# Kernel optimization log

Hardware: AMD Instinct MI355X
Metric: run time of the kernel (lower is better)

Reference implementation:

```python
import jax, jax.numpy as jnp
import numpy as np

DIM = 1024
NUM_HEADS = 16
HEAD_DIM = DIM // NUM_HEADS
BATCH = 2
SEQ = 2048
ROPE_BASE = 10000.0


def _rope_cos_sin(seq_len, head_dim, dtype=jnp.float32):
    inv_freq = 1.0 / (ROPE_BASE ** (jnp.arange(0, head_dim, 2, dtype=jnp.float32) / head_dim))
    t = jnp.arange(seq_len, dtype=jnp.float32)
    freqs = jnp.outer(t, inv_freq)              # (S, D/2)
    emb = jnp.concatenate([freqs, freqs], axis=-1)  # (S, D)
    return jnp.cos(emb).astype(dtype), jnp.sin(emb).astype(dtype)


def _rotate_half(x):
    x1, x2 = jnp.split(x, 2, axis=-1)
    return jnp.concatenate([-x2, x1], axis=-1)


def _apply_rope(x, cos, sin):
    # x: (B, S, H, D); cos/sin: (S, D) -> broadcast (1, S, 1, D)
    cos = cos[None, :, None, :]
    sin = sin[None, :, None, :]
    return x * cos + _rotate_half(x) * sin


def setup_inputs() -> dict:
    key = jax.random.key(0)
    ks = jax.random.split(key, 5)
    x = jax.random.normal(ks[0], (BATCH, SEQ, DIM), dtype=jnp.float32)
    scale = DIM ** -0.5
    wq = jax.random.normal(ks[1], (DIM, DIM), dtype=jnp.float32) * scale
    wk = jax.random.normal(ks[2], (DIM, DIM), dtype=jnp.float32) * scale
    wv = jax.random.normal(ks[3], (DIM, DIM), dtype=jnp.float32) * scale
    wo = jax.random.normal(ks[4], (DIM, DIM), dtype=jnp.float32) * scale
    return {"x": x, "wq": wq, "wk": wk, "wv": wv, "wo": wo}


def reference(x, wq, wk, wv, wo):
    B, S, _ = x.shape
    scale = HEAD_DIM ** -0.5
    # nn.Linear(x) = x @ W.T; weights stored (out, in)
    q = (x @ wq.T).reshape(B, S, NUM_HEADS, HEAD_DIM)
    k = (x @ wk.T).reshape(B, S, NUM_HEADS, HEAD_DIM)
    v = (x @ wv.T).reshape(B, S, NUM_HEADS, HEAD_DIM)
    cos, sin = _rope_cos_sin(S, HEAD_DIM, x.dtype)
    q = _apply_rope(q, cos, sin)
    k = _apply_rope(k, cos, sin)
    # (B, H, S, S) scores, full softmax attention (no mask, dropout=0)
    scores = jnp.einsum('bqhd,bkhd->bhqk', q, k) * scale
    attn = jax.nn.softmax(scores, axis=-1)
    out = jnp.einsum('bhqk,bkhd->bqhd', attn, v).reshape(B, S, DIM)
    return out @ wo.T
```

## Files before the change

kernel.cpp:

```cpp
#include <hip/hip_runtime.h>
#include <hip/hip_bf16.h>
#include <stdint.h>


#define AS1(p) ((const __attribute__((address_space(1))) void*)(p))
#define AS3(p) ((__attribute__((address_space(3))) void*)(p))

typedef __attribute__((ext_vector_type(8)))  __bf16 bf16x8;
typedef __attribute__((ext_vector_type(4)))  float  f32x4;
typedef __attribute__((ext_vector_type(16))) float  f32x16;

__device__ __forceinline__ ushort f2b(float f) {
  union { float f; uint32_t u; } v; v.f = f;
  uint32_t u = v.u;
  u += 0x7fffu + ((u >> 16) & 1);
  return (ushort)(u >> 16);
}
__device__ __forceinline__ float b2f(ushort s) {
  union { uint32_t u; float f; } v; v.u = ((uint32_t)s) << 16;
  return v.f;
}
__device__ __forceinline__ uint32_t pkbf16(float lo, float hi) {
  uint32_t w;
  asm("v_cvt_pk_bf16_f32 %0, %1, %2" : "=v"(w) : "v"(lo), "v"(hi));
  return w;
}
__device__ __forceinline__ float fast_exp2(float x) {
#if __has_builtin(__builtin_amdgcn_exp2f)
  return __builtin_amdgcn_exp2f(x);
#else
  float r;
  asm("v_exp_f32 %0, %1\n\ts_nop 1" : "=v"(r) : "v"(x));
  return r;
#endif
}

__global__ __launch_bounds__(256) void cvt_all_k(
    const float* __restrict__ x,  const float* __restrict__ wq,
    const float* __restrict__ wk, const float* __restrict__ wv,
    const float* __restrict__ wo, ushort* __restrict__ dst) {
  int i = blockIdx.x * 256 + threadIdx.x;
  const float* src;
  if      (i < 1048576) src = x  + (size_t)i * 4;
  else if (i < 1310720) src = wq + (size_t)(i - 1048576) * 4;
  else if (i < 1572864) src = wk + (size_t)(i - 1310720) * 4;
  else if (i < 1835008) src = wv + (size_t)(i - 1572864) * 4;
  else                  src = wo + (size_t)(i - 1835008) * 4;
  float4 v = *(const float4*)src;
  ushort4 o;
  o.x = f2b(v.x); o.y = f2b(v.y); o.z = f2b(v.z); o.w = f2b(v.w);
  ((ushort4*)dst)[i] = o;
}

__device__ __forceinline__ void gemm_mainloop(
    const ushort* __restrict__ A, const ushort* __restrict__ W,
    int row0, int col0, ushort* lds, f32x4 acc[4][4]) {
  const int K = 1024;
  int tid = threadIdx.x;
  int lane = tid & 63, wid = tid >> 6;
  int wr = wid >> 1, wc = wid & 1;
  int lr = lane >> 4, lc = lane & 15;
  ushort* lA = lds;
  ushort* lB = lds + 8192;

  auto stage = [&](int buf, int k0) {
#pragma unroll
    for (int i = 0; i < 2; i++) {
      int idx = tid + i * 256;
      const ushort* ga = A + (size_t)(row0 + (idx >> 2)) * K + k0 + (idx & 3) * 8;
      __builtin_amdgcn_global_load_lds(AS1(ga),
          AS3(lA + buf * 4096 + (i * 256 + wid * 64) * 8), 16, 0, 0);
      const ushort* gb = W + (size_t)(col0 + (idx >> 2)) * K + k0 + (idx & 3) * 8;
      __builtin_amdgcn_global_load_lds(AS1(gb),
          AS3(lB + buf * 4096 + (i * 256 + wid * 64) * 8), 16, 0, 0);
    }
  };

  stage(0, 0);
  __syncthreads();
  int cur = 0;
  for (int k0 = 0; k0 < K; k0 += 32) {
    if (k0 + 32 < K) stage(cur ^ 1, k0 + 32);
    const ushort* a  = lA + cur * 4096;
    const ushort* bm = lB + cur * 4096;
    bf16x8 af[4], bfr[4];
#pragma unroll
    for (int m = 0; m < 4; m++)
      af[m] = *(const bf16x8*)(a + (wr * 64 + m * 16 + lc) * 32 + lr * 8);
#pragma unroll
    for (int n = 0; n < 4; n++)
      bfr[n] = *(const bf16x8*)(bm + (wc * 64 + n * 16 + lc) * 32 + lr * 8);
#pragma unroll
    for (int m = 0; m < 4; m++)
#pragma unroll
      for (int n = 0; n < 4; n++)
        acc[m][n] = __builtin_amdgcn_mfma_f32_16x16x32_bf16(af[m], bfr[n], acc[m][n], 0, 0, 0);
    __syncthreads();
    cur ^= 1;
  }
}

__global__ __launch_bounds__(256) void gemm_qkv_k(
    const ushort* __restrict__ xb,
    const ushort* __restrict__ wqb, const ushort* __restrict__ wkb,
    const ushort* __restrict__ wvb,
    ushort* __restrict__ Qb, ushort* __restrict__ Kb, ushort* __restrict__ Vtb) {
  __shared__ ushort lds[16384];
  int z = blockIdx.z;
  const ushort* w = (z == 0) ? wqb : (z == 1) ? wkb : wvb;
  int row0 = blockIdx.x * 128, col0 = blockIdx.y * 128;
  f32x4 acc[4][4] = {};
  gemm_mainloop(xb, w, row0, col0, lds, acc);

  int tid = threadIdx.x, lane = tid & 63, wid = tid >> 6;
  int wr = wid >> 1, wc = wid & 1, lr = lane >> 4, lc = lane & 15;

  if (z < 2) {
    ushort* dst = (z == 0) ? Qb : Kb;
#pragma unroll
    for (int m = 0; m < 4; m++)
#pragma unroll
      for (int n = 0; n < 4; n++)
#pragma unroll
        for (int j = 0; j < 4; j++) {
          int i = row0 + wr * 64 + m * 16 + lr * 4 + j;
          int c = col0 + wc * 64 + n * 16 + lc;
          int b = i >> 11, s = i & 2047, h = c >> 6, d = c & 63;
          dst[(size_t)(b * 16 + h) * 131072 + (size_t)s * 64 + d] = f2b(acc[m][n][j]);
        }
  } else {
#pragma unroll
    for (int m = 0; m < 4; m++)
#pragma unroll
      for (int n = 0; n < 4; n++) {
        int c = wc * 64 + n * 16 + lc;
        int sb = wr * 64 + m * 16 + lr * 4;
        uint32_t w0 = pkbf16(acc[m][n][0], acc[m][n][1]);
        uint32_t w1 = pkbf16(acc[m][n][2], acc[m][n][3]);
        int soff = sb ^ ((c & 7) << 3);
        uint2 val; val.x = w0; val.y = w1;
        *(uint2*)(lds + c * 128 + soff) = val;
      }
    __syncthreads();
    int b = row0 >> 11, srow = row0 & 2047;
#pragma unroll
    for (int i = 0; i < 8; i++) {
      int idx = i * 256 + tid;
      int cl = idx >> 4, sc = idx & 15;
      int soff = (sc * 8) ^ ((cl & 7) << 3);
      bf16x8 v = *(const bf16x8*)(lds + cl * 128 + soff);
      int cg = col0 + cl, h = cg >> 6, d = cg & 63;
      *(bf16x8*)(Vtb + (size_t)(b * 16 + h) * 131072 + (size_t)d * 2048 + srow + sc * 8) = v;
    }
  }
}

__global__ __launch_bounds__(256) void gemm_out_k(
    const ushort* __restrict__ Ab, const ushort* __restrict__ wob,
    float* __restrict__ out) {
  __shared__ ushort lds[16384];
  int row0 = blockIdx.x * 128, col0 = blockIdx.y * 128;
  f32x4 acc[4][4] = {};
  gemm_mainloop(Ab, wob, row0, col0, lds, acc);

  int tid = threadIdx.x, lane = tid & 63, wid = tid >> 6;
  int wr = wid >> 1, wc = wid & 1, lr = lane >> 4, lc = lane & 15;
#pragma unroll
  for (int m = 0; m < 4; m++)
#pragma unroll
    for (int n = 0; n < 4; n++)
#pragma unroll
      for (int j = 0; j < 4; j++) {
        int i = row0 + wr * 64 + m * 16 + lr * 4 + j;
        int c = col0 + wc * 64 + n * 16 + lc;
        out[(size_t)i * 1024 + c] = acc[m][n][j];
      }
}

__global__ __launch_bounds__(256) void rope_k(ushort* __restrict__ Qb,
                                              ushort* __restrict__ Kb) {
  const float QSCL = 0.125f * 1.44269504088896f;
  int idx = blockIdx.x * 256 + threadIdx.x;
  int dp = idx & 31;
  int s  = (idx >> 5) & 2047;
  int bh = idx >> 16;
  float inv = exp2f((float)dp * (-13.2877123795494f / 32.0f));
  float ang = (float)s * inv;
  float sn, cs;
  sincosf(ang, &sn, &cs);
  size_t off = (size_t)bh * 131072 + (size_t)s * 64 + dp;
  float q1 = b2f(Qb[off]), q2 = b2f(Qb[off + 32]);
  Qb[off]      = f2b((q1 * cs - q2 * sn) * QSCL);
  Qb[off + 32] = f2b((q2 * cs + q1 * sn) * QSCL);
  float k1 = b2f(Kb[off]), k2 = b2f(Kb[off + 32]);
  Kb[off]      = f2b(k1 * cs - k2 * sn);
  Kb[off + 32] = f2b(k2 * cs + k1 * sn);
}

__global__ __launch_bounds__(512, 4) void attn_k(
    const ushort* __restrict__ Qb, const ushort* __restrict__ Kb,
    const ushort* __restrict__ Vtb, ushort* __restrict__ Ob) {
  __shared__ char ldsb[65536];
  int tid = threadIdx.x, lane = tid & 63, wid = tid >> 6;
  int lc5 = lane & 31, hi = lane >> 5;
  int qsub = wid & 3, grp = wid >> 2;

  int bid = blockIdx.x;
  int qt = (bid >> 3) & 15;
  int bh = (bid & 7) + ((bid >> 7) << 3);
  int q0 = qt * 128 + qsub * 32;
  const ushort* Qp = Qb  + (size_t)bh * 131072 + (size_t)q0 * 64;
  const ushort* Kp = Kb  + (size_t)bh * 131072;
  const ushort* Vp = Vtb + (size_t)bh * 131072;

  bf16x8 qf[4];
#pragma unroll
  for (int ks = 0; ks < 4; ks++)
    qf[ks] = *(const bf16x8*)(Qp + lc5 * 64 + ks * 16 + hi * 8);

  f32x16 o0, o1;
#pragma unroll
  for (int i = 0; i < 16; i++) { o0[i] = 0.f; o1[i] = 0.f; }
  float lsum = 0.f;

  int swz[4];
#pragma unroll
  for (int ks = 0; ks < 4; ks++)
    swz[ks] = (((2 * ks + hi) ^ (lc5 & 7)) << 4);
  const int rbase = lc5 * 128;

  auto stage = [&](int buf, int kvp) {
    int r = tid >> 3, cp = tid & 7;
    int ubase = wid * 1024;
#pragma unroll
    for (int t = 0; t < 2; t++) {
      char* tb = ldsb + buf * 32768 + t * 16384;
      const ushort* gk = Kp + (size_t)(kvp + 64 * t + r) * 64 + ((cp ^ (r & 7)) << 3);
      __builtin_amdgcn_global_load_lds(AS1(gk), AS3(tb + ubase), 16, 0, 0);
      const ushort* gv = Vp + (size_t)r * 2048 + kvp + 64 * t + ((cp ^ (r & 7)) << 3);
      __builtin_amdgcn_global_load_lds(AS1(gv), AS3(tb + 8192 + ubase), 16, 0, 0);
    }
  };

  stage(0, 0);
  stage(1, 128);
  int cur = 0;

  for (int kvp = 0; kvp < 2048; kvp += 128) {
    if (kvp + 128 < 2048) asm volatile("s_waitcnt vmcnt(4)" ::: "memory");
    else                  asm volatile("s_waitcnt vmcnt(0)" ::: "memory");
    asm volatile("s_barrier" ::: "memory");

    const char* kbuf = ldsb + cur * 32768 + grp * 16384;
    const char* vbuf = kbuf + 8192;

    f32x16 s0 = {}, s1 = {};
    __builtin_amdgcn_s_setprio(1);
#pragma unroll
    for (int ks = 0; ks < 4; ks++) {
      bf16x8 ka0 = *(const bf16x8*)(kbuf + rbase + swz[ks]);
      bf16x8 ka1 = *(const bf16x8*)(kbuf + 4096 + rbase + swz[ks]);
      s0 = __builtin_amdgcn_mfma_f32_32x32x16_bf16(ka0, qf[ks], s0, 0, 0, 0);
      s1 = __builtin_amdgcn_mfma_f32_32x32x16_bf16(ka1, qf[ks], s1, 0, 0, 0);
    }
    __builtin_amdgcn_s_setprio(0);

#pragma unroll
    for (int i = 0; i < 16; i++) {
      s0[i] = fast_exp2(s0[i]);
      s1[i] = fast_exp2(s1[i]);
    }
    float acc = 0.f;
#pragma unroll
    for (int i = 0; i < 16; i++) acc += s0[i] + s1[i];
    lsum += acc;

    bf16x8 a[4];
#pragma unroll
    for (int t = 0; t < 2; t++) {
      const f32x16& s = t ? s1 : s0;
#pragma unroll
      for (int h2 = 0; h2 < 2; h2++) {
        int rb = 8 * h2;
        uint32_t wa1 = pkbf16(s[rb],     s[rb + 1]);
        uint32_t wb1 = pkbf16(s[rb + 4], s[rb + 5]);
        asm("v_permlane32_swap_b32 %0, %1" : "+v"(wa1), "+v"(wb1));
        uint32_t wa2 = pkbf16(s[rb + 2], s[rb + 3]);
        uint32_t wb2 = pkbf16(s[rb + 6], s[rb + 7]);
        asm("v_permlane32_swap_b32 %0, %1" : "+v"(wa2), "+v"(wb2));
        union { uint32_t u[4]; bf16x8 v; } tmp;
        tmp.u[0] = wa1; tmp.u[1] = wa2; tmp.u[2] = wb1; tmp.u[3] = wb2;
        a[t * 2 + h2] = tmp.v;
      }
    }

    __builtin_amdgcn_s_setprio(1);
#pragma unroll
    for (int ks = 0; ks < 4; ks++) {
      bf16x8 vb0 = *(const bf16x8*)(vbuf + rbase + swz[ks]);
      bf16x8 vb1 = *(const bf16x8*)(vbuf + 4096 + rbase + swz[ks]);
      o0 = __builtin_amdgcn_mfma_f32_32x32x16_bf16(a[ks], vb0, o0, 0, 0, 0);
      o1 = __builtin_amdgcn_mfma_f32_32x32x16_bf16(a[ks], vb1, o1, 0, 0, 0);
    }
    __builtin_amdgcn_s_setprio(0);

    asm volatile("s_barrier" ::: "memory");
    if (kvp + 256 < 2048) stage(cur, kvp + 256);
    cur ^= 1;
  }

  float* cb = (float*)ldsb;
  float* p = cb + (size_t)(qsub * 64 + lane) * 33;
  if (grp == 1) {
#pragma unroll
    for (int i = 0; i < 16; i++) { p[i] = o0[i]; p[16 + i] = o1[i]; }
    p[32] = lsum;
  }
  __syncthreads();
  if (grp == 0) {
#pragma unroll
    for (int i = 0; i < 16; i++) { o0[i] += p[i]; o1[i] += p[16 + i]; }
    lsum += p[32];

    lsum += __shfl_xor(lsum, 32);
    float invq = 1.0f / lsum;
    float invr[16];
#pragma unroll
    for (int r = 0; r < 16; r++)
      invr[r] = __shfl(invq, (r & 3) + 8 * (r >> 2) + 4 * hi);

    int b = bh >> 4, h = bh & 15;
    ushort* Op = Ob + (size_t)(b * 2048 + q0) * 1024 + h * 64 + lc5;
#pragma unroll
    for (int r = 0; r < 16; r++) {
      int rrow = (r & 3) + 8 * (r >> 2) + 4 * hi;
      Op[(size_t)rrow * 1024]      = f2b(o0[r] * invr[r]);
      Op[(size_t)rrow * 1024 + 32] = f2b(o1[r] * invr[r]);
    }
  }
}

extern "C" void kernel_launch(void* const* d_in, const int* in_sizes, int n_in,
                              void* d_out, int out_size, void* d_ws, size_t ws_size,
                              hipStream_t stream) {
  const float* x  = (const float*)d_in[0];
  const float* wq = (const float*)d_in[1];
  const float* wk = (const float*)d_in[2];
  const float* wv = (const float*)d_in[3];
  const float* wo = (const float*)d_in[4];
  float* out = (float*)d_out;
  char* ws = (char*)d_ws;
  const size_t MiB = 1024 * 1024;
  ushort* xb  = (ushort*)(ws + 0);
  ushort* wqb = (ushort*)(ws + 8 * MiB);
  ushort* wkb = (ushort*)(ws + 10 * MiB);
  ushort* wvb = (ushort*)(ws + 12 * MiB);
  ushort* wob = (ushort*)(ws + 14 * MiB);
  ushort* Qb  = (ushort*)(ws + 16 * MiB);
  ushort* Kb  = (ushort*)(ws + 24 * MiB);
  ushort* Vtb = (ushort*)(ws + 32 * MiB);
  ushort* Ob  = (ushort*)(ws + 40 * MiB);

  cvt_all_k<<<8192, 256, 0, stream>>>(x, wq, wk, wv, wo, xb);
  dim3 gqkv(32, 8, 3);
  gemm_qkv_k<<<gqkv, 256, 0, stream>>>(xb, wqb, wkb, wvb, Qb, Kb, Vtb);
  rope_k<<<8192, 256, 0, stream>>>(Qb, Kb);
  attn_k<<<512, 512, 0, stream>>>(Qb, Kb, Vtb, Ob);
  dim3 gout(32, 8);
  gemm_out_k<<<gout, 256, 0, stream>>>(Ob, wob, out);
}
```

Before: 110.1 us.

## Fuse RoPE into QKV GEMM epilogue using precomputed cos/sin table

```diff
diff --git a/kernel.cpp b/kernel.cpp
--- a/kernel.cpp
+++ b/kernel.cpp
@@ -38,7 +38,8 @@
 __global__ __launch_bounds__(256) void cvt_all_k(
     const float* __restrict__ x,  const float* __restrict__ wq,
     const float* __restrict__ wk, const float* __restrict__ wv,
-    const float* __restrict__ wo, ushort* __restrict__ dst) {
+    const float* __restrict__ wo, ushort* __restrict__ dst,
+    float2* __restrict__ tab) {
   int i = blockIdx.x * 256 + threadIdx.x;
   const float* src;
   if      (i < 1048576) src = x  + (size_t)i * 4;
@@ -50,6 +51,15 @@
   ushort4 o;
   o.x = f2b(v.x); o.y = f2b(v.y); o.z = f2b(v.z); o.w = f2b(v.w);
   ((ushort4*)dst)[i] = o;
+
+  if (i < 65536) {
+    int s = i >> 5, dp = i & 31;
+    float inv = exp2f((float)dp * (-13.2877123795494f / 32.0f));
+    float ang = (float)s * inv;
+    float sn, cs;
+    sincosf(ang, &sn, &cs);
+    tab[i] = make_float2(cs, sn);
+  }
 }
 
 __device__ __forceinline__ void gemm_mainloop(
@@ -104,6 +114,7 @@
     const ushort* __restrict__ xb,
     const ushort* __restrict__ wqb, const ushort* __restrict__ wkb,
     const ushort* __restrict__ wvb,
+    const float2* __restrict__ tab,
     ushort* __restrict__ Qb, ushort* __restrict__ Kb, ushort* __restrict__ Vtb) {
   __shared__ ushort lds[16384];
   int z = blockIdx.z;
@@ -117,16 +128,23 @@
 
   if (z < 2) {
     ushort* dst = (z == 0) ? Qb : Kb;
+    const float qs = (z == 0) ? 0.125f * 1.44269504088896f : 1.0f;
 #pragma unroll
     for (int m = 0; m < 4; m++)
 #pragma unroll
-      for (int n = 0; n < 4; n++)
+      for (int n = 0; n < 2; n++)
 #pragma unroll
         for (int j = 0; j < 4; j++) {
           int i = row0 + wr * 64 + m * 16 + lr * 4 + j;
           int c = col0 + wc * 64 + n * 16 + lc;
-          int b = i >> 11, s = i & 2047, h = c >> 6, d = c & 63;
-          dst[(size_t)(b * 16 + h) * 131072 + (size_t)s * 64 + d] = f2b(acc[m][n][j]);
+          int b = i >> 11, s = i & 2047, h = c >> 6, dp = c & 31;
+          float2 cs = tab[s * 32 + dp];
+          float q1 = acc[m][n][j], q2 = acc[m][n + 2][j];
+          float r1 = (q1 * cs.x - q2 * cs.y) * qs;
+          float r2 = (q2 * cs.x + q1 * cs.y) * qs;
+          size_t base = (size_t)(b * 16 + h) * 131072 + (size_t)s * 64;
+          dst[base + dp]      = f2b(r1);
+          dst[base + dp + 32] = f2b(r2);
         }
   } else {
 #pragma unroll
@@ -175,26 +193,6 @@
         int c = col0 + wc * 64 + n * 16 + lc;
         out[(size_t)i * 1024 + c] = acc[m][n][j];
       }
-}
-
-__global__ __launch_bounds__(256) void rope_k(ushort* __restrict__ Qb,
-                                              ushort* __restrict__ Kb) {
-  const float QSCL = 0.125f * 1.44269504088896f;
-  int idx = blockIdx.x * 256 + threadIdx.x;
-  int dp = idx & 31;
-  int s  = (idx >> 5) & 2047;
-  int bh = idx >> 16;
-  float inv = exp2f((float)dp * (-13.2877123795494f / 32.0f));
-  float ang = (float)s * inv;
-  float sn, cs;
-  sincosf(ang, &sn, &cs);
-  size_t off = (size_t)bh * 131072 + (size_t)s * 64 + dp;
-  float q1 = b2f(Qb[off]), q2 = b2f(Qb[off + 32]);
-  Qb[off]      = f2b((q1 * cs - q2 * sn) * QSCL);
-  Qb[off + 32] = f2b((q2 * cs + q1 * sn) * QSCL);
-  float k1 = b2f(Kb[off]), k2 = b2f(Kb[off + 32]);
-  Kb[off]      = f2b(k1 * cs - k2 * sn);
-  Kb[off + 32] = f2b(k2 * cs + k1 * sn);
 }
 
 __global__ __launch_bounds__(512, 4) void attn_k(
@@ -360,11 +358,11 @@
   ushort* Kb  = (ushort*)(ws + 24 * MiB);
   ushort* Vtb = (ushort*)(ws + 32 * MiB);
   ushort* Ob  = (ushort*)(ws + 40 * MiB);
-
-  cvt_all_k<<<8192, 256, 0, stream>>>(x, wq, wk, wv, wo, xb);
+  float2* tab = (float2*)Ob;
+
+  cvt_all_k<<<8192, 256, 0, stream>>>(x, wq, wk, wv, wo, xb, tab);
   dim3 gqkv(32, 8, 3);
-  gemm_qkv_k<<<gqkv, 256, 0, stream>>>(xb, wqb, wkb, wvb, Qb, Kb, Vtb);
-  rope_k<<<8192, 256, 0, stream>>>(Qb, Kb);
+  gemm_qkv_k<<<gqkv, 256, 0, stream>>>(xb, wqb, wkb, wvb, tab, Qb, Kb, Vtb);
   attn_k<<<512, 512, 0, stream>>>(Qb, Kb, Vtb, Ob);
   dim3 gout(32, 8);
   gemm_out_k<<<gout, 256, 0, stream>>>(Ob, wob, out);
```

New measurement: 103.9 us. -5.7%, faster.
